# Performance work log

Measured on AMD Instinct MI355X. Metric: run time of the kernel, lower is better.

## Reference

```python
import jax, jax.numpy as jnp
import numpy as np

B, N, D = 256, 64, 3
MSG_IN = 3 * D + 2   # [x_i, x_j, r, |r|, |r|^2] = 11
MSG_H = 128
HID = 128


def setup_inputs() -> dict:
    key = jax.random.key(0)
    ks = jax.random.split(key, 16)
    def lin(k, fin, fout):
        k1, k2 = jax.random.split(k)
        lim = 1.0 / np.sqrt(fin)
        w = jax.random.uniform(k1, (fin, fout), jnp.float32, -lim, lim)
        b = jax.random.uniform(k2, (fout,), jnp.float32, -lim, lim)
        return w, b
    phi_w1, phi_b1 = lin(ks[0], MSG_IN, MSG_H)
    phi_w2, phi_b2 = lin(ks[1], MSG_H, MSG_H)
    psi_w1, psi_b1 = lin(ks[2], D + MSG_H, HID)
    psi_w2, psi_b2 = lin(ks[3], HID, HID)
    psi_w3, psi_b3 = lin(ks[4], HID, D)
    x = jax.random.normal(ks[5], (B, N, D), jnp.float32)
    spin = jax.random.randint(ks[6], (N,), 0, 2, jnp.int64 if jax.config.jax_enable_x64 else jnp.int32)
    bf_scale = jnp.float32(0.05)
    return {"x": x, "spin": spin,
            "phi_w1": phi_w1, "phi_b1": phi_b1, "phi_w2": phi_w2, "phi_b2": phi_b2,
            "psi_w1": psi_w1, "psi_b1": psi_b1, "psi_w2": psi_w2, "psi_b2": psi_b2,
            "psi_w3": psi_w3, "psi_b3": psi_b3, "bf_scale": bf_scale}


def reference(x, spin, phi_w1, phi_b1, phi_w2, phi_b2,
              psi_w1, psi_b1, psi_w2, psi_b2, psi_w3, psi_b3, bf_scale):
    b, n, d = x.shape
    r = x[:, :, None, :] - x[:, None, :, :]              # (B,N,N,d)
    r2 = jnp.sum(r * r, axis=-1, keepdims=True)          # (B,N,N,1)
    r1 = jnp.sqrt(r2 + 1e-12)
    xi = jnp.broadcast_to(x[:, :, None, :], (b, n, n, d))
    xj = jnp.broadcast_to(x[:, None, :, :], (b, n, n, d))
    msg_in = jnp.concatenate([xi, xj, r, r1, r2], axis=-1)  # (B,N,N,3d+2)
    # use_spin=True, same_spin_only=False -> mask is all-ones (spin unused)
    eye = jnp.eye(n, dtype=x.dtype)[None, :, :, None]
    mask = 1.0 - eye                                      # zero out self-messages
    h = jax.nn.silu(msg_in @ phi_w1 + phi_b1)
    m_ij = jax.nn.silu(h @ phi_w2 + phi_b2)              # (B,N,N,msg_hidden)
    m_i = jnp.sum(m_ij * mask, axis=2)                   # (B,N,msg_hidden)
    upd = jnp.concatenate([x, m_i], axis=-1)
    u = jax.nn.silu(upd @ psi_w1 + psi_b1)
    u = jax.nn.silu(u @ psi_w2 + psi_b2)
    dx = u @ psi_w3 + psi_b3
    return jnp.tanh(dx) * jnp.maximum(bf_scale, 0.0)
```

## Files before the change

### kernel.cpp

```cpp
#include <hip/hip_runtime.h>
#include <math.h>

#define NT 256

typedef short bf16x8 __attribute__((ext_vector_type(8)));
typedef float f32x4 __attribute__((ext_vector_type(4)));

__device__ __forceinline__ float silu_f(float z) {
    return z / (1.0f + __expf(-z));
}
__device__ __forceinline__ unsigned short f2bf(float f) {
    unsigned int u = __float_as_uint(f);
    u += 0x7FFFu + ((u >> 16) & 1u);
    return (unsigned short)(u >> 16);
}
__device__ __forceinline__ float bf2f(unsigned short s) {
    return __uint_as_float(((unsigned int)s) << 16);
}

__global__ __launch_bounds__(NT, 3) void backflow_kernel(
    const float* __restrict__ x,
    const float* __restrict__ phi_w1, const float* __restrict__ phi_b1,
    const float* __restrict__ phi_w2, const float* __restrict__ phi_b2,
    const float* __restrict__ psi_w1, const float* __restrict__ psi_b1,
    const float* __restrict__ psi_w2, const float* __restrict__ psi_b2,
    const float* __restrict__ psi_w3, const float* __restrict__ psi_b3,
    const float* __restrict__ bf_scale,
    float* __restrict__ out)
{
    __shared__ __align__(16) unsigned short A_hi[64 * 128];
    __shared__ __align__(16) unsigned short A_lo[64 * 128];
    __shared__ __align__(16) float x_l4[64 * 4];
    __shared__ __align__(16) float upd_l[8 * 132];
    __shared__ __align__(16) float u1_l[8 * 132];
    __shared__ float red_l[48];

    const int tid  = threadIdx.x;
    const int b    = blockIdx.x >> 3;
    const int i0   = (blockIdx.x & 7) * 8;
    const int wv   = tid >> 6;
    const int lane = tid & 63;
    const int lr   = lane & 15;
    const int lg   = lane >> 4;

    bf16x8 bh[2][4], bl[2][4];
    float b2c[2];
    #pragma unroll
    for (int c2 = 0; c2 < 2; ++c2) {
        const int ct = wv + 4 * c2;
        const int n  = ct * 16 + lr;
        b2c[c2] = phi_b2[n];
        #pragma unroll
        for (int ks = 0; ks < 4; ++ks) {
            #pragma unroll
            for (int e = 0; e < 8; ++e) {
                const int k = ks * 32 + lg * 8 + e;
                const float w = phi_w2[k * 128 + n];
                const unsigned short h = f2bf(w);
                bh[c2][ks][e] = (short)h;
                bl[c2][ks][e] = (short)f2bf(w - bf2f(h));
            }
        }
    }

    const int kq = (tid & 31) * 4;
    const int jg = tid >> 5;
    float w1r[44];
    #pragma unroll
    for (int d = 0; d < 11; ++d)
        #pragma unroll
        for (int kk = 0; kk < 4; ++kk)
            w1r[d * 4 + kk] = phi_w1[d * 128 + kq + kk];
    float b1r[4];
    #pragma unroll
    for (int kk = 0; kk < 4; ++kk) b1r[kk] = phi_b1[kq + kk];

    if (tid < 64) {
        x_l4[tid * 4 + 0] = x[b * 192 + tid * 3 + 0];
        x_l4[tid * 4 + 1] = x[b * 192 + tid * 3 + 1];
        x_l4[tid * 4 + 2] = x[b * 192 + tid * 3 + 2];
        x_l4[tid * 4 + 3] = 0.0f;
    }
    __syncthreads();

    #pragma unroll 1
    for (int il = 0; il < 8; ++il) {
        const int i = i0 + il;
        const float xi0 = x_l4[i * 4 + 0], xi1 = x_l4[i * 4 + 1], xi2 = x_l4[i * 4 + 2];
        float preb[4];
        #pragma unroll
        for (int kk = 0; kk < 4; ++kk)
            preb[kk] = b1r[kk] + xi0 * w1r[0 + kk] + xi1 * w1r[4 + kk] + xi2 * w1r[8 + kk];

        #pragma unroll
        for (int jj = 0; jj < 8; ++jj) {
            const int j = jg * 8 + jj;
            const float4 xj4 = *(const float4*)&x_l4[j * 4];
            const float r0 = xi0 - xj4.x, r1 = xi1 - xj4.y, r2 = xi2 - xj4.z;
            const float r2s = r0 * r0 + r1 * r1 + r2 * r2;
            const float rn  = sqrtf(r2s + 1e-12f);
            unsigned short hh[4], ll[4];
            #pragma unroll
            for (int kk = 0; kk < 4; ++kk) {
                const float p = preb[kk]
                    + xj4.x * w1r[12 + kk] + xj4.y * w1r[16 + kk] + xj4.z * w1r[20 + kk]
                    + r0 * w1r[24 + kk] + r1 * w1r[28 + kk] + r2 * w1r[32 + kk]
                    + rn * w1r[36 + kk] + r2s * w1r[40 + kk];
                const float h = silu_f(p);
                hh[kk] = f2bf(h);
                ll[kk] = f2bf(h - bf2f(hh[kk]));
            }
            const int byte = ((j * 128 + kq) * 2) ^ ((j & 7) << 4);
            *(ushort4*)((char*)A_hi + byte) = make_ushort4(hh[0], hh[1], hh[2], hh[3]);
            *(ushort4*)((char*)A_lo + byte) = make_ushort4(ll[0], ll[1], ll[2], ll[3]);
        }
        __syncthreads();

        if (tid < 3) upd_l[il * 132 + tid] = x_l4[i * 4 + tid];
        float msum0 = 0.0f, msum1 = 0.0f;
        const int a_base = lr * 256 + lg * 16;
        const int a_swz  = (lr & 7) << 4;
        #pragma unroll
        for (int jt = 0; jt < 4; ++jt) {
            bf16x8 ah[4], al[4];
            #pragma unroll
            for (int ks = 0; ks < 4; ++ks) {
                const int off = (jt * 4096 + ks * 64 + a_base) ^ a_swz;
                ah[ks] = *(const bf16x8*)((const char*)A_hi + off);
                al[ks] = *(const bf16x8*)((const char*)A_lo + off);
            }
            #pragma unroll
            for (int c2 = 0; c2 < 2; ++c2) {
                f32x4 acc = {0.0f, 0.0f, 0.0f, 0.0f};
                #pragma unroll
                for (int ks = 0; ks < 4; ++ks) {
                    acc = __builtin_amdgcn_mfma_f32_16x16x32_bf16(ah[ks], bh[c2][ks], acc, 0, 0, 0);
                    acc = __builtin_amdgcn_mfma_f32_16x16x32_bf16(al[ks], bh[c2][ks], acc, 0, 0, 0);
                    acc = __builtin_amdgcn_mfma_f32_16x16x32_bf16(ah[ks], bl[c2][ks], acc, 0, 0, 0);
                }
                #pragma unroll
                for (int v = 0; v < 4; ++v) {
                    const int row = jt * 16 + lg * 4 + v;
                    const float mv = silu_f(acc[v] + b2c[c2]);
                    const float add = (row == i) ? 0.0f : mv;
                    if (c2 == 0) msum0 += add; else msum1 += add;
                }
            }
        }
        msum0 += __shfl_xor(msum0, 16, 64); msum0 += __shfl_xor(msum0, 32, 64);
        msum1 += __shfl_xor(msum1, 16, 64); msum1 += __shfl_xor(msum1, 32, 64);
        if (lane < 16) {
            upd_l[il * 132 + 3 + (wv) * 16 + lr]     = msum0;
            upd_l[il * 132 + 3 + (wv + 4) * 16 + lr] = msum1;
        }
        __syncthreads();
    }

    const int c   = tid & 127;
    const int rep = tid >> 7;
    const int n0  = rep * 4;
    float a4[4];
    const float pb1 = psi_b1[c];
    #pragma unroll
    for (int nn = 0; nn < 4; ++nn) a4[nn] = pb1;
    for (int k = 0; k < 131; ++k) {
        const float w = psi_w1[k * 128 + c];
        #pragma unroll
        for (int nn = 0; nn < 4; ++nn) a4[nn] += upd_l[(n0 + nn) * 132 + k] * w;
    }
    #pragma unroll
    for (int nn = 0; nn < 4; ++nn) u1_l[(n0 + nn) * 132 + c] = silu_f(a4[nn]);
    __syncthreads();

    const float pb2 = psi_b2[c];
    #pragma unroll
    for (int nn = 0; nn < 4; ++nn) a4[nn] = pb2;
    for (int k = 0; k < 128; ++k) {
        const float w = psi_w2[k * 128 + c];
        #pragma unroll
        for (int nn = 0; nn < 4; ++nn) a4[nn] += u1_l[(n0 + nn) * 132 + k] * w;
    }
    float u2[4];
    #pragma unroll
    for (int nn = 0; nn < 4; ++nn) u2[nn] = silu_f(a4[nn]);

    const float w30 = psi_w3[c * 3 + 0];
    const float w31 = psi_w3[c * 3 + 1];
    const float w32 = psi_w3[c * 3 + 2];
    float pd[4][3];
    #pragma unroll
    for (int nn = 0; nn < 4; ++nn) {
        pd[nn][0] = u2[nn] * w30;
        pd[nn][1] = u2[nn] * w31;
        pd[nn][2] = u2[nn] * w32;
    }
    #pragma unroll
    for (int off = 32; off > 0; off >>= 1) {
        #pragma unroll
        for (int nn = 0; nn < 4; ++nn) {
            pd[nn][0] += __shfl_xor(pd[nn][0], off, 64);
            pd[nn][1] += __shfl_xor(pd[nn][1], off, 64);
            pd[nn][2] += __shfl_xor(pd[nn][2], off, 64);
        }
    }
    if (lane == 0) {
        #pragma unroll
        for (int nn = 0; nn < 4; ++nn) {
            red_l[wv * 12 + nn * 3 + 0] = pd[nn][0];
            red_l[wv * 12 + nn * 3 + 1] = pd[nn][1];
            red_l[wv * 12 + nn * 3 + 2] = pd[nn][2];
        }
    }
    __syncthreads();
    if (tid < 24) {
        const int n = tid / 3, d = tid % 3;
        const int wa = (n < 4) ? 0 : 2;
        const float dx = red_l[wa * 12 + (n & 3) * 3 + d]
                       + red_l[(wa + 1) * 12 + (n & 3) * 3 + d] + psi_b3[d];
        out[(b * 64 + i0 + n) * 3 + d] = tanhf(dx) * fmaxf(bf_scale[0], 0.0f);
    }
}

extern "C" void kernel_launch(void* const* d_in, const int* in_sizes, int n_in,
                              void* d_out, int out_size, void* d_ws, size_t ws_size,
                              hipStream_t stream) {
    const float* x        = (const float*)d_in[0];
    const float* phi_w1   = (const float*)d_in[2];
    const float* phi_b1   = (const float*)d_in[3];
    const float* phi_w2   = (const float*)d_in[4];
    const float* phi_b2   = (const float*)d_in[5];
    const float* psi_w1   = (const float*)d_in[6];
    const float* psi_b1   = (const float*)d_in[7];
    const float* psi_w2   = (const float*)d_in[8];
    const float* psi_b2   = (const float*)d_in[9];
    const float* psi_w3   = (const float*)d_in[10];
    const float* psi_b3   = (const float*)d_in[11];
    const float* bf_scale = (const float*)d_in[12];
    float* out = (float*)d_out;

    backflow_kernel<<<dim3(2048), dim3(NT), 0, stream>>>(
        x, phi_w1, phi_b1, phi_w2, phi_b2,
        psi_w1, psi_b1, psi_w2, psi_b2, psi_w3, psi_b3,
        bf_scale, out);
}
```

Before: 296.5 us.

## Double-buffer layer-1 activations to overlap next row's compute with MFMA stage

Splits the per-row loop into a prologue plus a software-pipelined loop. Each iteration computes the first MLP layer for row i+1 into a second LDS buffer while the MFMA second layer consumes row i, which removes one barrier per row. LDS usage doubles, so launch bounds drop from 3 to 2 blocks per CU, and u1_l now aliases the A_hi buffer to save shared memory. It also adds unroll-by-4 pragmas to the psi GEMV loops.

```diff
diff --git a/kernel.cpp b/kernel.cpp
--- a/kernel.cpp
+++ b/kernel.cpp
@@ -18,7 +18,7 @@
     return __uint_as_float(((unsigned int)s) << 16);
 }
 
-__global__ __launch_bounds__(NT, 3) void backflow_kernel(
+__global__ __launch_bounds__(NT, 2) void backflow_kernel(
     const float* __restrict__ x,
     const float* __restrict__ phi_w1, const float* __restrict__ phi_b1,
     const float* __restrict__ phi_w2, const float* __restrict__ phi_b2,
@@ -28,11 +28,10 @@
     const float* __restrict__ bf_scale,
     float* __restrict__ out)
 {
-    __shared__ __align__(16) unsigned short A_hi[64 * 128];
-    __shared__ __align__(16) unsigned short A_lo[64 * 128];
+    __shared__ __align__(16) unsigned short A_hi[2 * 64 * 128];
+    __shared__ __align__(16) unsigned short A_lo[2 * 64 * 128];
     __shared__ __align__(16) float x_l4[64 * 4];
     __shared__ __align__(16) float upd_l[8 * 132];
-    __shared__ __align__(16) float u1_l[8 * 132];
     __shared__ float red_l[48];
 
     const int tid  = threadIdx.x;
@@ -83,15 +82,13 @@
     }
     __syncthreads();
 
-    #pragma unroll 1
-    for (int il = 0; il < 8; ++il) {
-        const int i = i0 + il;
+    {
+        const int i = i0;
         const float xi0 = x_l4[i * 4 + 0], xi1 = x_l4[i * 4 + 1], xi2 = x_l4[i * 4 + 2];
         float preb[4];
         #pragma unroll
         for (int kk = 0; kk < 4; ++kk)
             preb[kk] = b1r[kk] + xi0 * w1r[0 + kk] + xi1 * w1r[4 + kk] + xi2 * w1r[8 + kk];
-
         #pragma unroll
         for (int jj = 0; jj < 8; ++jj) {
             const int j = jg * 8 + jj;
@@ -114,18 +111,57 @@
             *(ushort4*)((char*)A_hi + byte) = make_ushort4(hh[0], hh[1], hh[2], hh[3]);
             *(ushort4*)((char*)A_lo + byte) = make_ushort4(ll[0], ll[1], ll[2], ll[3]);
         }
-        __syncthreads();
+    }
+    __syncthreads();
+
+    #pragma unroll 1
+    for (int il = 0; il < 8; ++il) {
+        const int i = i0 + il;
+        const int curb = (il & 1) * 16384;
+        const int nxtb = curb ^ 16384;
 
         if (tid < 3) upd_l[il * 132 + tid] = x_l4[i * 4 + tid];
+
+        if (il < 7) {
+            const int i2 = i + 1;
+            const float yi0 = x_l4[i2 * 4 + 0], yi1 = x_l4[i2 * 4 + 1], yi2 = x_l4[i2 * 4 + 2];
+            float preb[4];
+            #pragma unroll
+            for (int kk = 0; kk < 4; ++kk)
+                preb[kk] = b1r[kk] + yi0 * w1r[0 + kk] + yi1 * w1r[4 + kk] + yi2 * w1r[8 + kk];
+            #pragma unroll
+            for (int jj = 0; jj < 8; ++jj) {
+                const int j = jg * 8 + jj;
+                const float4 xj4 = *(const float4*)&x_l4[j * 4];
+                const float r0 = yi0 - xj4.x, r1 = yi1 - xj4.y, r2 = yi2 - xj4.z;
+                const float r2s = r0 * r0 + r1 * r1 + r2 * r2;
+                const float rn  = sqrtf(r2s + 1e-12f);
+                unsigned short hh[4], ll[4];
+                #pragma unroll
+                for (int kk = 0; kk < 4; ++kk) {
+                    const float p = preb[kk]
+                        + xj4.x * w1r[12 + kk] + xj4.y * w1r[16 + kk] + xj4.z * w1r[20 + kk]
+                        + r0 * w1r[24 + kk] + r1 * w1r[28 + kk] + r2 * w1r[32 + kk]
+                        + rn * w1r[36 + kk] + r2s * w1r[40 + kk];
+                    const float h = silu_f(p);
+                    hh[kk] = f2bf(h);
+                    ll[kk] = f2bf(h - bf2f(hh[kk]));
+                }
+                const int byte = nxtb + (((j * 128 + kq) * 2) ^ ((j & 7) << 4));
+                *(ushort4*)((char*)A_hi + byte) = make_ushort4(hh[0], hh[1], hh[2], hh[3]);
+                *(ushort4*)((char*)A_lo + byte) = make_ushort4(ll[0], ll[1], ll[2], ll[3]);
+            }
+        }
+
         float msum0 = 0.0f, msum1 = 0.0f;
-        const int a_base = lr * 256 + lg * 16;
+        const int a_base = curb + lr * 256 + lg * 16;
         const int a_swz  = (lr & 7) << 4;
         #pragma unroll
         for (int jt = 0; jt < 4; ++jt) {
             bf16x8 ah[4], al[4];
             #pragma unroll
             for (int ks = 0; ks < 4; ++ks) {
-                const int off = (jt * 4096 + ks * 64 + a_base) ^ a_swz;
+                const int off = ((jt * 4096 + ks * 64 + a_base) ^ a_swz);
                 ah[ks] = *(const bf16x8*)((const char*)A_hi + off);
                 al[ks] = *(const bf16x8*)((const char*)A_lo + off);
             }
@@ -156,6 +192,8 @@
         __syncthreads();
     }
 
+    float* u1_l = (float*)A_hi;
+
     const int c   = tid & 127;
     const int rep = tid >> 7;
     const int n0  = rep * 4;
@@ -163,6 +201,7 @@
     const float pb1 = psi_b1[c];
     #pragma unroll
     for (int nn = 0; nn < 4; ++nn) a4[nn] = pb1;
+    #pragma unroll 4
     for (int k = 0; k < 131; ++k) {
         const float w = psi_w1[k * 128 + c];
         #pragma unroll
@@ -175,6 +214,7 @@
     const float pb2 = psi_b2[c];
     #pragma unroll
     for (int nn = 0; nn < 4; ++nn) a4[nn] = pb2;
+    #pragma unroll 4
     for (int k = 0; k < 128; ++k) {
         const float w = psi_w2[k * 128 + c];
         #pragma unroll
```

Measured after the change: 277.6 us. 1.07x faster.
